# Performance work log

Measured on AMD Instinct MI355X. Metric: run time of the kernel, lower is better.

## Reference

```python
import jax, jax.numpy as jnp
import numpy as np
from jax import lax

K = 3
PAD = 1
STRIDE = 1
DIL = 1
BN_EPS = 1e-5


def bilinear_gather(x, py, px):
    """Zero-padded bilinear sampling. x:[B,C,Hin,Win]; py,px:[B,T,H,W] -> [B,C,T,H,W]."""
    B, C, Hin, Win = x.shape
    xf = x.reshape(B, C, Hin * Win)
    y0 = jnp.floor(py)
    x0 = jnp.floor(px)
    wy1 = py - y0
    wx1 = px - x0
    wy0 = 1.0 - wy1
    wx0 = 1.0 - wx1

    def corner(yc, xc, w):
        valid = (yc >= 0) & (yc <= Hin - 1) & (xc >= 0) & (xc <= Win - 1)
        yi = jnp.clip(yc, 0, Hin - 1).astype(jnp.int32)
        xi = jnp.clip(xc, 0, Win - 1).astype(jnp.int32)
        idx = (yi * Win + xi).reshape(B, -1)  # [B, T*H*W]
        vals = jax.vmap(lambda xb, ib: xb[:, ib])(xf, idx)  # [B, C, T*H*W]
        vals = vals.reshape(B, C, *py.shape[1:])
        return vals * (w * valid.astype(x.dtype))[:, None]

    return (corner(y0, x0, wy0 * wx0) + corner(y0, x0 + 1.0, wy0 * wx1)
            + corner(y0 + 1.0, x0, wy1 * wx0) + corner(y0 + 1.0, x0 + 1.0, wy1 * wx1))


def setup_inputs() -> dict:
    key = jax.random.key(0)
    ks = jax.random.split(key, 6)
    B, C, H, W, O = 8, 128, 80, 80, 128
    x = jax.random.normal(ks[0], (B, C, H, W), dtype=jnp.float32)
    # offset/mask conv (zero-init in the module; small random here so sampling is exercised)
    w_off = jax.random.normal(ks[1], (3 * K * K, C, K, K), dtype=jnp.float32) * 0.05
    b_off = jax.random.normal(ks[2], (3 * K * K,), dtype=jnp.float32) * 0.01
    # main DCN weight: uniform(-std, std), std = 1/sqrt(C*K*K)
    std = 1.0 / float(np.sqrt(C * K * K))
    w_dcn = jax.random.uniform(ks[3], (O, C, K, K), dtype=jnp.float32, minval=-std, maxval=std)
    b_dcn = jax.random.normal(ks[4], (O,), dtype=jnp.float32) * 0.01
    gamma = jnp.ones((O,), dtype=jnp.float32)
    beta = jnp.zeros((O,), dtype=jnp.float32)
    return {"x": x, "w_dcn": w_dcn, "b_dcn": b_dcn, "w_off": w_off, "b_off": b_off,
            "gamma": gamma, "beta": beta}


def reference(x, w_dcn, b_dcn, w_off, b_off, gamma, beta):
    B, C, H, W = x.shape
    O = w_dcn.shape[0]
    # offset/mask conv (k=3, s=1, p=1) -> [B, 27, H, W]
    om = lax.conv_general_dilated(x, w_off, (STRIDE, STRIDE), [(PAD, PAD), (PAD, PAD)],
                                  dimension_numbers=("NCHW", "OIHW", "NCHW"))
    om = om + b_off[None, :, None, None]
    o1, o2, m = jnp.split(om, 3, axis=1)  # each [B, 9, H, W]
    mask = jax.nn.sigmoid(m)
    # torch: offset = cat(o1, o2); torchvision reads channel 2t as dy_t, 2t+1 as dx_t
    off = jnp.concatenate([o1, o2], axis=1).reshape(B, K * K, 2, H, W)
    dy, dx = off[:, :, 0], off[:, :, 1]  # [B, 9, H, W]
    ky, kx = jnp.meshgrid(jnp.arange(K), jnp.arange(K), indexing="ij")
    ky = ky.reshape(-1)
    kx = kx.reshape(-1)  # [9]
    base_y = (jnp.arange(H)[None, :, None] * STRIDE - PAD + ky[:, None, None] * DIL).astype(x.dtype)  # [9,H,1]
    base_x = (jnp.arange(W)[None, None, :] * STRIDE - PAD + kx[:, None, None] * DIL).astype(x.dtype)  # [9,1,W]
    py = dy + base_y[None]  # [B, 9, H, W]
    px = dx + base_x[None]
    sampled = bilinear_gather(x, py, px)  # [B, C, 9, H, W]
    sampled = sampled * mask[:, None]  # modulated (dg=1 broadcasts over C)
    wk = w_dcn.reshape(O, C, K * K)
    out = jnp.einsum("bckhw,ock->bohw", sampled, wk) + b_dcn[None, :, None, None]
    # BatchNorm (training-mode batch stats, biased variance) + SiLU
    mu = out.mean(axis=(0, 2, 3), keepdims=True)
    var = out.var(axis=(0, 2, 3), keepdims=True)
    y = (out - mu) * lax.rsqrt(var + BN_EPS) * gamma[None, :, None, None] + beta[None, :, None, None]
    return y * jax.nn.sigmoid(y)
```

## Files before the change

kernel.cpp:

```cpp
#include <hip/hip_runtime.h>
#include <hip/hip_bf16.h>

constexpr int B = 8, C = 128, H = 80, W = 80, O = 128;
constexpr int HW = H * W;
constexpr int NPIX = B * HW;
constexpr int KC = C * 9;
constexpr int PX = 32;
constexpr int NBLK = NPIX / PX;

typedef __attribute__((ext_vector_type(8))) short short8;
typedef __attribute__((ext_vector_type(4))) float f32x4;

__device__ inline ushort f2b(float f) {
  uint u = __float_as_uint(f);
  return (ushort)((u + 0x7FFFu + ((u >> 16) & 1u)) >> 16);
}
__device__ inline void unp(uint u, float& lo, float& hi) {
  lo = __uint_as_float(u << 16);
  hi = __uint_as_float(u & 0xFFFF0000u);
}
__device__ inline uint pk2(float lo, float hi) {
  __hip_bfloat162 h = __float22bfloat162_rn(make_float2(lo, hi));
  return *reinterpret_cast<uint*>(&h);
}
__device__ inline int swz16(int px, int byte) {
  return (px * 256 + (byte ^ ((px & 7) << 4))) >> 1;
}

__global__ __launch_bounds__(256) void k_xt(const float* __restrict__ x,
                                            ushort* __restrict__ xt) {
  const int t = threadIdx.x;
  const int g = t >> 4;
  const int hl = t & 15;
  const int p0 = blockIdx.x * 16;
  const int b = p0 / HW, hw = p0 - b * HW + hl;
  const float* xb = x + (size_t)b * C * HW + hw;
  uint u[4];
#pragma unroll
  for (int i = 0; i < 4; ++i) {
    float lo = xb[(size_t)(g * 8 + 2 * i) * HW];
    float hi = xb[(size_t)(g * 8 + 2 * i + 1) * HW];
    u[i] = (uint)f2b(lo) | ((uint)f2b(hi) << 16);
  }
  *(uint4*)(xt + ((size_t)b * HW + hw) * C + g * 8) = make_uint4(u[0], u[1], u[2], u[3]);
}

__global__ __launch_bounds__(256) void k_wt2(const float* __restrict__ w_dcn,
                                             const float* __restrict__ w_off,
                                             ushort* __restrict__ wt,
                                             ushort* __restrict__ wof,
                                             ushort* __restrict__ zrow) {
  int i = blockIdx.x * 256 + threadIdx.x;
  if (i < O * KC) {
    int c = i & 127, k = (i >> 7) % 9, o = i / KC;
    wt[i] = f2b(w_dcn[(size_t)o * KC + c * 9 + k]);
  }
  if (i < 32 * KC) {
    int c = i & 127, k = (i >> 7) % 9, o = i / KC;
    wof[i] = (o < 27) ? f2b(w_off[((size_t)o * C + c) * 9 + k]) : (ushort)0;
  }
  if (i < 128) zrow[i] = 0;
}

__global__ __launch_bounds__(256, 6) void k_offc4(
    const ushort* __restrict__ xt, const ushort* __restrict__ wof,
    const ushort* __restrict__ zrow, const float* __restrict__ b_off,
    float* __restrict__ om) {
  const int t = threadIdx.x;
  const int bid = (blockIdx.x & 7) * 200 + (blockIdx.x >> 3);
  const int b = bid / 200, hw0 = (bid - b * 200) * PX;
  const int lane = t & 63, wv = t >> 6, rl = lane & 15, gh = lane >> 4;
  const int mi = wv & 1, nt = wv >> 1;
  const int px = hw0 + nt * 16 + rl;
  const int hp = px / W, wp = px - hp * W;
  const ushort* xb = xt + (size_t)b * HW * C;
  f32x4 acc = {0.f, 0.f, 0.f, 0.f};
#pragma unroll
  for (int k = 0; k < 9; ++k) {
    int ky = k / 3, kx = k - ky * 3;
    int y = hp + ky - 1, xx = wp + kx - 1;
    bool ok = ((unsigned)y < (unsigned)H) && ((unsigned)xx < (unsigned)W);
    const ushort* rowp = ok ? (xb + (size_t)(y * W + xx) * C) : zrow;
    const ushort* aP = wof + (size_t)(mi * 16 + rl) * KC + k * 128 + gh * 8;
#pragma unroll
    for (int kk = 0; kk < 4; ++kk) {
      short8 av = *(const short8*)(aP + kk * 32);
      short8 bv = *(const short8*)(rowp + kk * 32 + gh * 8);
      acc = __builtin_amdgcn_mfma_f32_16x16x32_bf16(av, bv, acc, 0, 0, 0);
    }
  }
  float* ob = om + (size_t)b * 27 * HW + hw0 + nt * 16 + rl;
#pragma unroll
  for (int r = 0; r < 4; ++r) {
    int oc = mi * 16 + gh * 4 + r;
    if (oc < 27) ob[(size_t)oc * HW] = acc[r] + b_off[oc];
  }
}

__global__ __launch_bounds__(256, 4) void k_dcn3(
    const ushort* __restrict__ xt, const float* __restrict__ om,
    const ushort* __restrict__ wt, float* __restrict__ outr,
    float* __restrict__ part2) {
  __shared__ float s_w[PX][9][4];
  __shared__ int s_i[PX][9][4];
  __shared__ __align__(16) ushort s_buf[2][PX * 128];
  const int t = threadIdx.x;
  const int bid = (blockIdx.x & 7) * 200 + (blockIdx.x >> 3);
  const int b = bid / 200, hw0 = (bid - b * 200) * PX;

  for (int idx = t; idx < PX * 9; idx += 256) {
    int px = idx / 9, k = idx - (idx / 9) * 9;
    int hw = hw0 + px, h = hw / W, w = hw - (hw / W) * W;
    int ky = k / 3, kx = k - ky * 3;
    const float* omp = om + (size_t)b * 27 * HW + hw;
    float dy = omp[(size_t)(2 * k) * HW];
    float dx = omp[(size_t)(2 * k + 1) * HW];
    float mk = 1.0f / (1.0f + __expf(-omp[(size_t)(18 + k) * HW]));
    float py = dy + (float)(h - 1 + ky);
    float pxf = dx + (float)(w - 1 + kx);
    float y0f = floorf(py), x0f = floorf(pxf);
    float wy1 = py - y0f, wx1 = pxf - x0f;
    float wy0 = 1.0f - wy1, wx0 = 1.0f - wx1;
    int y0 = (int)y0f, x0 = (int)x0f;
    int y1 = y0 + 1, x1 = x0 + 1;
    bool vy0 = (y0 >= 0) && (y0 < H);
    bool vy1 = (y1 >= 0) && (y1 < H);
    bool vx0 = (x0 >= 0) && (x0 < W);
    bool vx1 = (x1 >= 0) && (x1 < W);
    int cy0 = min(max(y0, 0), H - 1), cy1 = min(max(y1, 0), H - 1);
    int cx0 = min(max(x0, 0), W - 1), cx1 = min(max(x1, 0), W - 1);
    s_w[px][k][0] = (vy0 && vx0) ? wy0 * wx0 * mk : 0.0f;
    s_w[px][k][1] = (vy0 && vx1) ? wy0 * wx1 * mk : 0.0f;
    s_w[px][k][2] = (vy1 && vx0) ? wy1 * wx0 * mk : 0.0f;
    s_w[px][k][3] = (vy1 && vx1) ? wy1 * wx1 * mk : 0.0f;
    s_i[px][k][0] = cy0 * W + cx0;
    s_i[px][k][1] = cy0 * W + cx1;
    s_i[px][k][2] = cy1 * W + cx0;
    s_i[px][k][3] = cy1 * W + cx1;
  }
  __syncthreads();

  const int sp = t >> 3, sq = t & 7;
  const ushort* xbq = xt + (size_t)b * HW * C + sq * 16;
  uint4 lA0, lA1, lB0, lB1, lC0, lC1, lD0, lD1;
  float cw0, cw1, cw2, cw3;

  auto SLOAD = [&](int k) {
    int4 ii = *(const int4*)&s_i[sp][k][0];
    float4 wf = *(const float4*)&s_w[sp][k][0];
    cw0 = wf.x; cw1 = wf.y; cw2 = wf.z; cw3 = wf.w;
    const ushort* r0 = xbq + (size_t)ii.x * C;
    const ushort* r1 = xbq + (size_t)ii.y * C;
    const ushort* r2 = xbq + (size_t)ii.z * C;
    const ushort* r3 = xbq + (size_t)ii.w * C;
    asm volatile("global_load_dwordx4 %0, %2, off\n\t"
                 "global_load_dwordx4 %1, %2, off offset:16"
                 : "=&v"(lA0), "=&v"(lA1) : "v"(r0));
    asm volatile("global_load_dwordx4 %0, %2, off\n\t"
                 "global_load_dwordx4 %1, %2, off offset:16"
                 : "=&v"(lB0), "=&v"(lB1) : "v"(r1));
    asm volatile("global_load_dwordx4 %0, %2, off\n\t"
                 "global_load_dwordx4 %1, %2, off offset:16"
                 : "=&v"(lC0), "=&v"(lC1) : "v"(r2));
    asm volatile("global_load_dwordx4 %0, %2, off\n\t"
                 "global_load_dwordx4 %1, %2, off offset:16"
                 : "=&v"(lD0), "=&v"(lD1) : "v"(r3));
  };

  auto SWRITE = [&](ushort* buf) {
    uint qa[8] = {lA0.x, lA0.y, lA0.z, lA0.w, lA1.x, lA1.y, lA1.z, lA1.w};
    uint qb[8] = {lB0.x, lB0.y, lB0.z, lB0.w, lB1.x, lB1.y, lB1.z, lB1.w};
    uint qc[8] = {lC0.x, lC0.y, lC0.z, lC0.w, lC1.x, lC1.y, lC1.z, lC1.w};
    uint qd[8] = {lD0.x, lD0.y, lD0.z, lD0.w, lD1.x, lD1.y, lD1.z, lD1.w};
    uint r[8];
#pragma unroll
    for (int d = 0; d < 8; ++d) {
      float a0, a1, b0, b1, c0, c1, d0, d1;
      unp(qa[d], a0, a1);
      unp(qb[d], b0, b1);
      unp(qc[d], c0, c1);
      unp(qd[d], d0, d1);
      float vlo = fmaf(cw3, d0, fmaf(cw2, c0, fmaf(cw1, b0, cw0 * a0)));
      float vhi = fmaf(cw3, d1, fmaf(cw2, c1, fmaf(cw1, b1, cw0 * a1)));
      r[d] = pk2(vlo, vhi);
    }
    *(uint4*)(buf + swz16(sp, sq * 32)) = make_uint4(r[0], r[1], r[2], r[3]);
    *(uint4*)(buf + swz16(sp, sq * 32 + 16)) = make_uint4(r[4], r[5], r[6], r[7]);
  };

  const int lane = t & 63, wv = t >> 6, rl = lane & 15, gh = lane >> 4;
  f32x4 acc00 = {0.f, 0.f, 0.f, 0.f}, acc01 = acc00, acc10 = acc00, acc11 = acc00;

  auto COMP = [&](const ushort* buf, int k) {
    const ushort* aP = wt + (size_t)(wv * 32 + rl) * KC + k * 128 + gh * 8;
    __builtin_amdgcn_s_setprio(1);
#pragma unroll
    for (int kk = 0; kk < 4; ++kk) {
      short8 av0 = *(const short8*)(aP + kk * 32);
      short8 av1 = *(const short8*)(aP + (size_t)16 * KC + kk * 32);
      short8 bv0 = *(const short8*)(buf + swz16(rl, kk * 64 + gh * 16));
      short8 bv1 = *(const short8*)(buf + swz16(16 + rl, kk * 64 + gh * 16));
      acc00 = __builtin_amdgcn_mfma_f32_16x16x32_bf16(av0, bv0, acc00, 0, 0, 0);
      acc01 = __builtin_amdgcn_mfma_f32_16x16x32_bf16(av0, bv1, acc01, 0, 0, 0);
      acc10 = __builtin_amdgcn_mfma_f32_16x16x32_bf16(av1, bv0, acc10, 0, 0, 0);
      acc11 = __builtin_amdgcn_mfma_f32_16x16x32_bf16(av1, bv1, acc11, 0, 0, 0);
    }
    __builtin_amdgcn_s_setprio(0);
  };

  SLOAD(0);
  asm volatile("s_waitcnt vmcnt(0)" ::: "memory");
  __builtin_amdgcn_sched_barrier(0);
  SWRITE(s_buf[0]);
  __syncthreads();
  for (int k = 0; k < 9; ++k) {
    if (k < 8) SLOAD(k + 1);
    COMP(s_buf[k & 1], k);
    __builtin_amdgcn_sched_barrier(0);
    if (k < 8) {
      asm volatile("s_waitcnt vmcnt(0)" ::: "memory");
      __builtin_amdgcn_sched_barrier(0);
      SWRITE(s_buf[(k + 1) & 1]);
      __syncthreads();
    }
  }

  float* outb = outr + (size_t)b * O * HW + hw0 + rl;
  const int nb = blockIdx.x;
#pragma unroll
  for (int mi = 0; mi < 2; ++mi) {
    f32x4 a0 = mi ? acc10 : acc00;
    f32x4 a1 = mi ? acc11 : acc01;
#pragma unroll
    for (int r = 0; r < 4; ++r) {
      int o = wv * 32 + mi * 16 + gh * 4 + r;
      outb[(size_t)o * HW] = a0[r];
      outb[(size_t)o * HW + 16] = a1[r];
      float s = a0[r] + a1[r];
      float s2 = fmaf(a0[r], a0[r], a1[r] * a1[r]);
#pragma unroll
      for (int m = 1; m < 16; m <<= 1) {
        s += __shfl_xor(s, m);
        s2 += __shfl_xor(s2, m);
      }
      if (rl == 0) {
        part2[(size_t)(2 * o) * NBLK + nb] = s;
        part2[(size_t)(2 * o + 1) * NBLK + nb] = s2;
      }
    }
  }
}

__global__ __launch_bounds__(256) void k_bnred(const float* __restrict__ part2,
                                               float* __restrict__ stats) {
  const int j = blockIdx.x;
  float s = 0.f;
  for (int i = threadIdx.x; i < NBLK; i += 256) s += part2[(size_t)j * NBLK + i];
#pragma unroll
  for (int off = 32; off > 0; off >>= 1) s += __shfl_down(s, off);
  __shared__ float rs[4];
  int wid = threadIdx.x >> 6, lane = threadIdx.x & 63;
  if (lane == 0) rs[wid] = s;
  __syncthreads();
  if (threadIdx.x == 0) stats[j] = rs[0] + rs[1] + rs[2] + rs[3];
}

__global__ __launch_bounds__(256) void k_bnapply2(
    float* __restrict__ outr, const float* __restrict__ stats,
    const float* __restrict__ gamma, const float* __restrict__ beta) {
  const int n4 = B * O * HW / 4;
  for (int i = blockIdx.x * blockDim.x + threadIdx.x; i < n4;
       i += gridDim.x * blockDim.x) {
    int o = (i / (HW / 4)) % O;
    float S = stats[2 * o], S2 = stats[2 * o + 1];
    const float inv = 1.0f / (float)(B * HW);
    float mu = S * inv;
    float rstd = rsqrtf(fmaf(S2, inv, -mu * mu) + 1e-5f);
    float a = rstd * gamma[o];
    float bb = fmaf(-mu, a, beta[o]);
    float4 v = ((const float4*)outr)[i];
    float y0 = fmaf(v.x, a, bb);
    float y1 = fmaf(v.y, a, bb);
    float y2 = fmaf(v.z, a, bb);
    float y3 = fmaf(v.w, a, bb);
    v.x = y0 / (1.0f + __expf(-y0));
    v.y = y1 / (1.0f + __expf(-y1));
    v.z = y2 / (1.0f + __expf(-y2));
    v.w = y3 / (1.0f + __expf(-y3));
    ((float4*)outr)[i] = v;
  }
}

extern "C" void kernel_launch(void* const* d_in, const int* in_sizes, int n_in,
                              void* d_out, int out_size, void* d_ws, size_t ws_size,
                              hipStream_t stream) {
  const float* x = (const float*)d_in[0];
  const float* w_dcn = (const float*)d_in[1];
  const float* w_off = (const float*)d_in[3];
  const float* b_off = (const float*)d_in[4];
  const float* gamma = (const float*)d_in[5];
  const float* beta = (const float*)d_in[6];
  float* out = (float*)d_out;
  float* om = (float*)d_ws;
  ushort* xt = (ushort*)(om + (size_t)B * 27 * HW);
  ushort* wt = xt + (size_t)B * HW * C;
  ushort* wof = wt + (size_t)O * KC;
  float* part2 = (float*)(wof + (size_t)32 * KC);
  float* stats = part2 + (size_t)256 * NBLK;
  ushort* zrow = (ushort*)(stats + 256);

  k_xt<<<NPIX / 16, 256, 0, stream>>>(x, xt);
  k_wt2<<<(O * KC + 255) / 256, 256, 0, stream>>>(w_dcn, w_off, wt, wof, zrow);
  k_offc4<<<NPIX / PX, 256, 0, stream>>>(xt, wof, zrow, b_off, om);
  k_dcn3<<<NPIX / PX, 256, 0, stream>>>(xt, om, wt, out, part2);
  k_bnred<<<256, 256, 0, stream>>>(part2, stats);
  k_bnapply2<<<2048, 256, 0, stream>>>(out, stats, gamma, beta);
}
```

Measured before the change: 245.3 us.

## Switch to fp16 with packed-half interpolation, 64-pixel DCN tiles, and LDS-transposed input

Converts the intermediate activations and weights from bf16 to fp16, so the bilinear blend can use packed half-precision multiply-adds instead of unpacking to fp32. The DCN kernel now processes 64 pixels per block with four N-tiles per wave, and loads the weight fragments into registers ahead of time, overlapped with the gather. The input transpose kernel stages data through swizzled LDS so global writes are coalesced. Risks include fp16 range and precision loss when blending in half, higher register pressure, and lower occupancy (launch bounds go from 4 to 3).

```diff
diff --git a/kernel.cpp b/kernel.cpp
--- a/kernel.cpp
+++ b/kernel.cpp
@@ -1,92 +1,97 @@
 #include <hip/hip_runtime.h>
 #include <hip/hip_bf16.h>
+#include <hip/hip_fp16.h>
 
 constexpr int B = 8, C = 128, H = 80, W = 80, O = 128;
 constexpr int HW = H * W;
 constexpr int NPIX = B * HW;
 constexpr int KC = C * 9;
-constexpr int PX = 32;
-constexpr int NBLK = NPIX / PX;
-
-typedef __attribute__((ext_vector_type(8))) short short8;
-typedef __attribute__((ext_vector_type(4))) float f32x4;
-
-__device__ inline ushort f2b(float f) {
-  uint u = __float_as_uint(f);
-  return (ushort)((u + 0x7FFFu + ((u >> 16) & 1u)) >> 16);
-}
-__device__ inline void unp(uint u, float& lo, float& hi) {
-  lo = __uint_as_float(u << 16);
-  hi = __uint_as_float(u & 0xFFFF0000u);
-}
-__device__ inline uint pk2(float lo, float hi) {
-  __hip_bfloat162 h = __float22bfloat162_rn(make_float2(lo, hi));
-  return *reinterpret_cast<uint*>(&h);
-}
-__device__ inline int swz16(int px, int byte) {
-  return (px * 256 + (byte ^ ((px & 7) << 4))) >> 1;
+constexpr int DPX = 64;
+constexpr int NBLK = NPIX / DPX;
+
+typedef _Float16 h8 __attribute__((ext_vector_type(8)));
+typedef _Float16 h2 __attribute__((ext_vector_type(2)));
+typedef float f32x4 __attribute__((ext_vector_type(4)));
+
+__device__ inline h8 as_h8(uint4 v) { h8 r; __builtin_memcpy(&r, &v, 16); return r; }
+__device__ inline h2 u2h(uint u) { h2 r; __builtin_memcpy(&r, &u, 4); return r; }
+__device__ inline uint h2u(h2 h) { uint r; __builtin_memcpy(&r, &h, 4); return r; }
+__device__ inline uint pkh(float a, float b) {
+  h2 h = { (_Float16)a, (_Float16)b };
+  return h2u(h);
+}
+__device__ inline int swz16(int row, int byte) {
+  return (row * 256 + (byte ^ ((row & 7) << 4))) >> 1;
 }
 
 __global__ __launch_bounds__(256) void k_xt(const float* __restrict__ x,
-                                            ushort* __restrict__ xt) {
+                                            _Float16* __restrict__ xt) {
+  __shared__ uint tile32[64 * 64];
   const int t = threadIdx.x;
-  const int g = t >> 4;
-  const int hl = t & 15;
-  const int p0 = blockIdx.x * 16;
-  const int b = p0 / HW, hw = p0 - b * HW + hl;
-  const float* xb = x + (size_t)b * C * HW + hw;
-  uint u[4];
-#pragma unroll
-  for (int i = 0; i < 4; ++i) {
-    float lo = xb[(size_t)(g * 8 + 2 * i) * HW];
-    float hi = xb[(size_t)(g * 8 + 2 * i + 1) * HW];
-    u[i] = (uint)f2b(lo) | ((uint)f2b(hi) << 16);
-  }
-  *(uint4*)(xt + ((size_t)b * HW + hw) * C + g * 8) = make_uint4(u[0], u[1], u[2], u[3]);
+  const int p0 = blockIdx.x * 64;
+  const int b = p0 / HW, hw0 = p0 - b * HW;
+  const int w = t >> 6, l = t & 63;
+#pragma unroll
+  for (int j = 0; j < 16; ++j) {
+    int c0 = (j * 4 + w) * 2;
+    float f0 = x[((size_t)(b * C + c0)) * HW + hw0 + l];
+    float f1 = x[((size_t)(b * C + c0 + 1)) * HW + hw0 + l];
+    int byte = l * 256 + ((c0 * 2) ^ ((l & 7) << 4));
+    tile32[byte >> 2] = pkh(f0, f1);
+  }
+  __syncthreads();
+  _Float16* dst = xt + (size_t)(b * HW + hw0) * C;
+#pragma unroll
+  for (int it = 0; it < 4; ++it) {
+    int g = w * 4096 + it * 1024 + l * 16;
+    int row = g >> 8, inner = g & 255;
+    uint4 v = *(const uint4*)((const char*)tile32 + row * 256 + (inner ^ ((row & 7) << 4)));
+    *(uint4*)(dst + (g >> 1)) = v;
+  }
 }
 
 __global__ __launch_bounds__(256) void k_wt2(const float* __restrict__ w_dcn,
                                              const float* __restrict__ w_off,
-                                             ushort* __restrict__ wt,
-                                             ushort* __restrict__ wof,
-                                             ushort* __restrict__ zrow) {
+                                             _Float16* __restrict__ wt,
+                                             _Float16* __restrict__ wof,
+                                             _Float16* __restrict__ zrow) {
   int i = blockIdx.x * 256 + threadIdx.x;
   if (i < O * KC) {
     int c = i & 127, k = (i >> 7) % 9, o = i / KC;
-    wt[i] = f2b(w_dcn[(size_t)o * KC + c * 9 + k]);
+    wt[i] = (_Float16)w_dcn[(size_t)o * KC + c * 9 + k];
   }
   if (i < 32 * KC) {
     int c = i & 127, k = (i >> 7) % 9, o = i / KC;
-    wof[i] = (o < 27) ? f2b(w_off[((size_t)o * C + c) * 9 + k]) : (ushort)0;
-  }
-  if (i < 128) zrow[i] = 0;
+    wof[i] = (o < 27) ? (_Float16)w_off[((size_t)o * C + c) * 9 + k] : (_Float16)0.f;
+  }
+  if (i < 128) zrow[i] = (_Float16)0.f;
 }
 
 __global__ __launch_bounds__(256, 6) void k_offc4(
-    const ushort* __restrict__ xt, const ushort* __restrict__ wof,
-    const ushort* __restrict__ zrow, const float* __restrict__ b_off,
+    const _Float16* __restrict__ xt, const _Float16* __restrict__ wof,
+    const _Float16* __restrict__ zrow, const float* __restrict__ b_off,
     float* __restrict__ om) {
   const int t = threadIdx.x;
   const int bid = (blockIdx.x & 7) * 200 + (blockIdx.x >> 3);
-  const int b = bid / 200, hw0 = (bid - b * 200) * PX;
+  const int b = bid / 200, hw0 = (bid - b * 200) * 32;
   const int lane = t & 63, wv = t >> 6, rl = lane & 15, gh = lane >> 4;
   const int mi = wv & 1, nt = wv >> 1;
   const int px = hw0 + nt * 16 + rl;
   const int hp = px / W, wp = px - hp * W;
-  const ushort* xb = xt + (size_t)b * HW * C;
+  const _Float16* xb = xt + (size_t)b * HW * C;
   f32x4 acc = {0.f, 0.f, 0.f, 0.f};
 #pragma unroll
   for (int k = 0; k < 9; ++k) {
     int ky = k / 3, kx = k - ky * 3;
     int y = hp + ky - 1, xx = wp + kx - 1;
     bool ok = ((unsigned)y < (unsigned)H) && ((unsigned)xx < (unsigned)W);
-    const ushort* rowp = ok ? (xb + (size_t)(y * W + xx) * C) : zrow;
-    const ushort* aP = wof + (size_t)(mi * 16 + rl) * KC + k * 128 + gh * 8;
+    const _Float16* rowp = ok ? (xb + (size_t)(y * W + xx) * C) : zrow;
+    const _Float16* aP = wof + (size_t)(mi * 16 + rl) * KC + k * 128 + gh * 8;
 #pragma unroll
     for (int kk = 0; kk < 4; ++kk) {
-      short8 av = *(const short8*)(aP + kk * 32);
-      short8 bv = *(const short8*)(rowp + kk * 32 + gh * 8);
-      acc = __builtin_amdgcn_mfma_f32_16x16x32_bf16(av, bv, acc, 0, 0, 0);
+      h8 av = *(const h8*)(aP + kk * 32);
+      h8 bv = *(const h8*)(rowp + kk * 32 + gh * 8);
+      acc = __builtin_amdgcn_mfma_f32_16x16x32_f16(av, bv, acc, 0, 0, 0);
     }
   }
   float* ob = om + (size_t)b * 27 * HW + hw0 + nt * 16 + rl;
@@ -97,18 +102,18 @@
   }
 }
 
-__global__ __launch_bounds__(256, 4) void k_dcn3(
-    const ushort* __restrict__ xt, const float* __restrict__ om,
-    const ushort* __restrict__ wt, float* __restrict__ outr,
+__global__ __launch_bounds__(256, 3) void k_dcn4(
+    const _Float16* __restrict__ xt, const float* __restrict__ om,
+    const _Float16* __restrict__ wt, float* __restrict__ outr,
     float* __restrict__ part2) {
-  __shared__ float s_w[PX][9][4];
-  __shared__ int s_i[PX][9][4];
-  __shared__ __align__(16) ushort s_buf[2][PX * 128];
+  __shared__ float s_w[DPX][9][4];
+  __shared__ int s_i[DPX][9][4];
+  __shared__ __align__(16) ushort s_buf[2][DPX * 128];
   const int t = threadIdx.x;
-  const int bid = (blockIdx.x & 7) * 200 + (blockIdx.x >> 3);
-  const int b = bid / 200, hw0 = (bid - b * 200) * PX;
-
-  for (int idx = t; idx < PX * 9; idx += 256) {
+  const int bid = (blockIdx.x & 7) * 100 + (blockIdx.x >> 3);
+  const int b = bid / 100, hw0 = (bid - b * 100) * DPX;
+
+  for (int idx = t; idx < DPX * 9; idx += 256) {
     int px = idx / 9, k = idx - (idx / 9) * 9;
     int hw = hw0 + px, h = hw / W, w = hw - (hw / W) * W;
     int ky = k / 3, kx = k - ky * 3;
@@ -140,104 +145,130 @@
   }
   __syncthreads();
 
-  const int sp = t >> 3, sq = t & 7;
-  const ushort* xbq = xt + (size_t)b * HW * C + sq * 16;
-  uint4 lA0, lA1, lB0, lB1, lC0, lC1, lD0, lD1;
+  const int sp = t >> 2, sq = t & 3;
+  const _Float16* xbq = xt + (size_t)b * HW * C + sq * 32;
+  const int lane = t & 63, wv = t >> 6, rl = lane & 15, gh = lane >> 4;
+  const _Float16* wbase = wt + (size_t)(wv * 32 + rl) * KC + gh * 8;
+
+  uint4 gA0, gA1, gA2, gA3, gB0, gB1, gB2, gB3;
+  uint4 gC0, gC1, gC2, gC3, gD0, gD1, gD2, gD3;
+  uint4 wA0, wA1, wA2, wA3, wB0, wB1, wB2, wB3;
   float cw0, cw1, cw2, cw3;
 
-  auto SLOAD = [&](int k) {
+#define GL4(o0, o1, o2, o3, P)                                            \
+  asm volatile("global_load_dwordx4 %0, %4, off\n\t"                      \
+               "global_load_dwordx4 %1, %4, off offset:16\n\t"            \
+               "global_load_dwordx4 %2, %4, off offset:32\n\t"            \
+               "global_load_dwordx4 %3, %4, off offset:48"                \
+               : "=&v"(o0), "=&v"(o1), "=&v"(o2), "=&v"(o3) : "v"(P))
+#define WL4(o0, o1, o2, o3, P)                                            \
+  asm volatile("global_load_dwordx4 %0, %4, off\n\t"                      \
+               "global_load_dwordx4 %1, %4, off offset:64\n\t"            \
+               "global_load_dwordx4 %2, %4, off offset:128\n\t"           \
+               "global_load_dwordx4 %3, %4, off offset:192"               \
+               : "=&v"(o0), "=&v"(o1), "=&v"(o2), "=&v"(o3) : "v"(P))
+
+  auto GLOAD = [&](int k) {
     int4 ii = *(const int4*)&s_i[sp][k][0];
     float4 wf = *(const float4*)&s_w[sp][k][0];
     cw0 = wf.x; cw1 = wf.y; cw2 = wf.z; cw3 = wf.w;
-    const ushort* r0 = xbq + (size_t)ii.x * C;
-    const ushort* r1 = xbq + (size_t)ii.y * C;
-    const ushort* r2 = xbq + (size_t)ii.z * C;
-    const ushort* r3 = xbq + (size_t)ii.w * C;
-    asm volatile("global_load_dwordx4 %0, %2, off\n\t"
-                 "global_load_dwordx4 %1, %2, off offset:16"
-                 : "=&v"(lA0), "=&v"(lA1) : "v"(r0));
-    asm volatile("global_load_dwordx4 %0, %2, off\n\t"
-                 "global_load_dwordx4 %1, %2, off offset:16"
-                 : "=&v"(lB0), "=&v"(lB1) : "v"(r1));
-    asm volatile("global_load_dwordx4 %0, %2, off\n\t"
-                 "global_load_dwordx4 %1, %2, off offset:16"
-                 : "=&v"(lC0), "=&v"(lC1) : "v"(r2));
-    asm volatile("global_load_dwordx4 %0, %2, off\n\t"
-                 "global_load_dwordx4 %1, %2, off offset:16"
-                 : "=&v"(lD0), "=&v"(lD1) : "v"(r3));
+    GL4(gA0, gA1, gA2, gA3, xbq + (size_t)ii.x * C);
+    GL4(gB0, gB1, gB2, gB3, xbq + (size_t)ii.y * C);
+    GL4(gC0, gC1, gC2, gC3, xbq + (size_t)ii.z * C);
+    GL4(gD0, gD1, gD2, gD3, xbq + (size_t)ii.w * C);
   };
+  auto WLOAD = [&](int k) {
+    const _Float16* a0 = wbase + k * 128;
+    WL4(wA0, wA1, wA2, wA3, a0);
+    WL4(wB0, wB1, wB2, wB3, a0 + 16 * KC);
+  };
 
   auto SWRITE = [&](ushort* buf) {
-    uint qa[8] = {lA0.x, lA0.y, lA0.z, lA0.w, lA1.x, lA1.y, lA1.z, lA1.w};
-    uint qb[8] = {lB0.x, lB0.y, lB0.z, lB0.w, lB1.x, lB1.y, lB1.z, lB1.w};
-    uint qc[8] = {lC0.x, lC0.y, lC0.z, lC0.w, lC1.x, lC1.y, lC1.z, lC1.w};
-    uint qd[8] = {lD0.x, lD0.y, lD0.z, lD0.w, lD1.x, lD1.y, lD1.z, lD1.w};
-    uint r[8];
-#pragma unroll
-    for (int d = 0; d < 8; ++d) {
-      float a0, a1, b0, b1, c0, c1, d0, d1;
-      unp(qa[d], a0, a1);
-      unp(qb[d], b0, b1);
-      unp(qc[d], c0, c1);
-      unp(qd[d], d0, d1);
-      float vlo = fmaf(cw3, d0, fmaf(cw2, c0, fmaf(cw1, b0, cw0 * a0)));
-      float vhi = fmaf(cw3, d1, fmaf(cw2, c1, fmaf(cw1, b1, cw0 * a1)));
-      r[d] = pk2(vlo, vhi);
+    uint qa[16] = {gA0.x, gA0.y, gA0.z, gA0.w, gA1.x, gA1.y, gA1.z, gA1.w,
+                   gA2.x, gA2.y, gA2.z, gA2.w, gA3.x, gA3.y, gA3.z, gA3.w};
+    uint qb[16] = {gB0.x, gB0.y, gB0.z, gB0.w, gB1.x, gB1.y, gB1.z, gB1.w,
+                   gB2.x, gB2.y, gB2.z, gB2.w, gB3.x, gB3.y, gB3.z, gB3.w};
+    uint qc[16] = {gC0.x, gC0.y, gC0.z, gC0.w, gC1.x, gC1.y, gC1.z, gC1.w,
+                   gC2.x, gC2.y, gC2.z, gC2.w, gC3.x, gC3.y, gC3.z, gC3.w};
+    uint qd[16] = {gD0.x, gD0.y, gD0.z, gD0.w, gD1.x, gD1.y, gD1.z, gD1.w,
+                   gD2.x, gD2.y, gD2.z, gD2.w, gD3.x, gD3.y, gD3.z, gD3.w};
+    h2 W0 = {(_Float16)cw0, (_Float16)cw0};
+    h2 W1 = {(_Float16)cw1, (_Float16)cw1};
+    h2 W2 = {(_Float16)cw2, (_Float16)cw2};
+    h2 W3 = {(_Float16)cw3, (_Float16)cw3};
+    uint r[16];
+#pragma unroll
+    for (int d = 0; d < 16; ++d) {
+      h2 o = u2h(qa[d]) * W0 + u2h(qb[d]) * W1 + u2h(qc[d]) * W2 + u2h(qd[d]) * W3;
+      r[d] = h2u(o);
     }
-    *(uint4*)(buf + swz16(sp, sq * 32)) = make_uint4(r[0], r[1], r[2], r[3]);
-    *(uint4*)(buf + swz16(sp, sq * 32 + 16)) = make_uint4(r[4], r[5], r[6], r[7]);
+#pragma unroll
+    for (int e = 0; e < 4; ++e)
+      *(uint4*)(buf + swz16(sp, sq * 64 + e * 16)) =
+          make_uint4(r[4 * e], r[4 * e + 1], r[4 * e + 2], r[4 * e + 3]);
   };
 
-  const int lane = t & 63, wv = t >> 6, rl = lane & 15, gh = lane >> 4;
-  f32x4 acc00 = {0.f, 0.f, 0.f, 0.f}, acc01 = acc00, acc10 = acc00, acc11 = acc00;
-
-  auto COMP = [&](const ushort* buf, int k) {
-    const ushort* aP = wt + (size_t)(wv * 32 + rl) * KC + k * 128 + gh * 8;
-    __builtin_amdgcn_s_setprio(1);
-#pragma unroll
-    for (int kk = 0; kk < 4; ++kk) {
-      short8 av0 = *(const short8*)(aP + kk * 32);
-      short8 av1 = *(const short8*)(aP + (size_t)16 * KC + kk * 32);
-      short8 bv0 = *(const short8*)(buf + swz16(rl, kk * 64 + gh * 16));
-      short8 bv1 = *(const short8*)(buf + swz16(16 + rl, kk * 64 + gh * 16));
-      acc00 = __builtin_amdgcn_mfma_f32_16x16x32_bf16(av0, bv0, acc00, 0, 0, 0);
-      acc01 = __builtin_amdgcn_mfma_f32_16x16x32_bf16(av0, bv1, acc01, 0, 0, 0);
-      acc10 = __builtin_amdgcn_mfma_f32_16x16x32_bf16(av1, bv0, acc10, 0, 0, 0);
-      acc11 = __builtin_amdgcn_mfma_f32_16x16x32_bf16(av1, bv1, acc11, 0, 0, 0);
-    }
-    __builtin_amdgcn_s_setprio(0);
+  f32x4 acc[2][4];
+#pragma unroll
+  for (int m = 0; m < 2; ++m)
+#pragma unroll
+    for (int nt = 0; nt < 4; ++nt) acc[m][nt] = {0.f, 0.f, 0.f, 0.f};
+
+  auto COMP = [&](const ushort* buf) {
+    h8 av0, av1, bv;
+#define KSTEP(WA, WB, KB)                                                  \
+  av0 = as_h8(WA); av1 = as_h8(WB);                                        \
+  _Pragma("unroll")                                                        \
+  for (int nt = 0; nt < 4; ++nt) {                                         \
+    bv = *(const h8*)(buf + swz16(nt * 16 + rl, KB + gh * 16));            \
+    acc[0][nt] = __builtin_amdgcn_mfma_f32_16x16x32_f16(av0, bv, acc[0][nt], 0, 0, 0); \
+    acc[1][nt] = __builtin_amdgcn_mfma_f32_16x16x32_f16(av1, bv, acc[1][nt], 0, 0, 0); \
+  }
+    KSTEP(wA0, wB0, 0)
+    KSTEP(wA1, wB1, 64)
+    KSTEP(wA2, wB2, 128)
+    KSTEP(wA3, wB3, 192)
+#undef KSTEP
   };
 
-  SLOAD(0);
-  asm volatile("s_waitcnt vmcnt(0)" ::: "memory");
+  GLOAD(0); WLOAD(0);
+  asm volatile("s_waitcnt vmcnt(8)" ::: "memory");
   __builtin_amdgcn_sched_barrier(0);
   SWRITE(s_buf[0]);
   __syncthreads();
+
   for (int k = 0; k < 9; ++k) {
-    if (k < 8) SLOAD(k + 1);
-    COMP(s_buf[k & 1], k);
+    if (k < 8) GLOAD(k + 1);
+    if (k < 8) asm volatile("s_waitcnt vmcnt(16)" ::: "memory");
+    else       asm volatile("s_waitcnt vmcnt(0)" ::: "memory");
     __builtin_amdgcn_sched_barrier(0);
+    COMP(s_buf[k & 1]);
     if (k < 8) {
-      asm volatile("s_waitcnt vmcnt(0)" ::: "memory");
+      WLOAD(k + 1);
+      asm volatile("s_waitcnt vmcnt(8)" ::: "memory");
       __builtin_amdgcn_sched_barrier(0);
       SWRITE(s_buf[(k + 1) & 1]);
       __syncthreads();
     }
   }
+#undef GL4
+#undef WL4
 
   float* outb = outr + (size_t)b * O * HW + hw0 + rl;
   const int nb = blockIdx.x;
 #pragma unroll
-  for (int mi = 0; mi < 2; ++mi) {
-    f32x4 a0 = mi ? acc10 : acc00;
-    f32x4 a1 = mi ? acc11 : acc01;
+  for (int mi = 0; mi < 2; ++mi)
 #pragma unroll
     for (int r = 0; r < 4; ++r) {
       int o = wv * 32 + mi * 16 + gh * 4 + r;
-      outb[(size_t)o * HW] = a0[r];
-      outb[(size_t)o * HW + 16] = a1[r];
-      float s = a0[r] + a1[r];
-      float s2 = fmaf(a0[r], a0[r], a1[r] * a1[r]);
+      float s = 0.f, s2 = 0.f;
+#pragma unroll
+      for (int nt = 0; nt < 4; ++nt) {
+        float v = acc[mi][nt][r];
+        outb[(size_t)o * HW + nt * 16] = v;
+        s += v;
+        s2 = fmaf(v, v, s2);
+      }
 #pragma unroll
       for (int m = 1; m < 16; m <<= 1) {
         s += __shfl_xor(s, m);
@@ -248,7 +279,6 @@
         part2[(size_t)(2 * o + 1) * NBLK + nb] = s2;
       }
     }
-  }
 }
 
 __global__ __launch_bounds__(256) void k_bnred(const float* __restrict__ part2,
@@ -302,17 +332,17 @@
   const float* beta = (const float*)d_in[6];
   float* out = (float*)d_out;
   float* om = (float*)d_ws;
-  ushort* xt = (ushort*)(om + (size_t)B * 27 * HW);
-  ushort* wt = xt + (size_t)B * HW * C;
-  ushort* wof = wt + (size_t)O * KC;
+  _Float16* xt = (_Float16*)(om + (size_t)B * 27 * HW);
+  _Float16* wt = xt + (size_t)B * HW * C;
+  _Float16* wof = wt + (size_t)O * KC;
   float* part2 = (float*)(wof + (size_t)32 * KC);
   float* stats = part2 + (size_t)256 * NBLK;
-  ushort* zrow = (ushort*)(stats + 256);
-
-  k_xt<<<NPIX / 16, 256, 0, stream>>>(x, xt);
+  _Float16* zrow = (_Float16*)(stats + 256);
+
+  k_xt<<<NPIX / 64, 256, 0, stream>>>(x, xt);
   k_wt2<<<(O * KC + 255) / 256, 256, 0, stream>>>(w_dcn, w_off, wt, wof, zrow);
-  k_offc4<<<NPIX / PX, 256, 0, stream>>>(xt, wof, zrow, b_off, om);
-  k_dcn3<<<NPIX / PX, 256, 0, stream>>>(xt, om, wt, out, part2);
+  k_offc4<<<NPIX / 32, 256, 0, stream>>>(xt, wof, zrow, b_off, om);
+  k_dcn4<<<NPIX / DPX, 256, 0, stream>>>(xt, om, wt, out, part2);
   k_bnred<<<256, 256, 0, stream>>>(part2, stats);
   k_bnapply2<<<2048, 256, 0, stream>>>(out, stats, gamma, beta);
 }
```

Result: faster. 230.5 us (-6.0%).
